# Performance work log

Measured on AMD Instinct MI355X. Metric: run time of the kernel, lower is better.

The kernel has to match this reference:

```python
import jax, jax.numpy as jnp
import numpy as np

B, T, C = 4, 2048, 1024
N_HEAD = 16
HEAD_DIM = C // N_HEAD

def setup_inputs() -> dict:
    key = jax.random.key(0)
    k1, k2, k3 = jax.random.split(key, 3)
    x = jax.random.normal(k1, (B, T, C), dtype=jnp.float32)
    # nn.Linear(C, 3C, bias=False): weight [3C, C], y = x @ W.T
    w_qkv = jax.random.normal(k2, (3 * C, C), dtype=jnp.float32) * (1.0 / np.sqrt(C))
    w_proj = jax.random.normal(k3, (C, C), dtype=jnp.float32) * (1.0 / np.sqrt(C))
    return {"x": x, "w_qkv": w_qkv, "w_proj": w_proj}

def reference(x, w_qkv, w_proj):
    Bx, Tx, Cx = x.shape
    qkv = x @ w_qkv.T  # [B,T,3C]
    q, k, v = jnp.split(qkv, 3, axis=-1)
    def heads(t):
        return t.reshape(Bx, Tx, N_HEAD, HEAD_DIM).transpose(0, 2, 1, 3)  # [B,H,T,D]
    q, k, v = heads(q), heads(k), heads(v)
    scale = HEAD_DIM ** -0.5
    att = jnp.einsum('bhtd,bhsd->bhts', q, k) * scale  # [B,H,T,T]
    causal = jnp.tril(jnp.ones((Tx, Tx), dtype=bool))
    att = jnp.where(causal[None, None], att, -jnp.inf)
    att = jax.nn.softmax(att, axis=-1)
    y = jnp.einsum('bhts,bhsd->bhtd', att, v)  # [B,H,T,D]
    y = y.transpose(0, 2, 1, 3).reshape(Bx, Tx, Cx)
    return y @ w_proj.T
```

## Files before the change

### kernel.cpp

```cpp
#include <hip/hip_runtime.h>
#include <hip/hip_bf16.h>

typedef __attribute__((ext_vector_type(8))) short bf16x8;
typedef __attribute__((ext_vector_type(4))) float f32x4;
typedef __attribute__((ext_vector_type(4))) unsigned short ushort4v;
typedef __attribute__((ext_vector_type(2))) unsigned uint2v;

__device__ __forceinline__ unsigned short f2bf(float f) {
  union { float f; unsigned u; } v; v.f = f;
  unsigned r = v.u + 0x7FFFu + ((v.u >> 16) & 1u);
  return (unsigned short)(r >> 16);
}

__device__ __forceinline__ unsigned pack_bf2(float lo, float hi) {
  __hip_bfloat162 h = __float22bfloat162_rn(make_float2(lo, hi));
  union { __hip_bfloat162 h; unsigned u; } cv; cv.h = h; return cv.u;
}

__device__ __forceinline__ void gll16(const void* g, void* l) {
  __builtin_amdgcn_global_load_lds((const __attribute__((address_space(1))) void*)g,
                                   (__attribute__((address_space(3))) void*)l, 16, 0, 0);
}

#define MFMA16(a, b, c) __builtin_amdgcn_mfma_f32_16x16x32_bf16((a), (b), (c), 0, 0, 0)

__global__ void cvt3(const float* __restrict__ x, const float* __restrict__ wq,
                     const float* __restrict__ wp,
                     unsigned short* __restrict__ xb, unsigned short* __restrict__ wqb,
                     unsigned short* __restrict__ wpb) {
  int i = (blockIdx.x * blockDim.x + threadIdx.x) * 4;
  const float* s; unsigned short* d;
  if (i < 8388608)        { s = x  + i;                 d = xb  + i; }
  else if (i < 11534336)  { s = wq + (i - 8388608);     d = wqb + (i - 8388608); }
  else                    { s = wp + (i - 11534336);    d = wpb + (i - 11534336); }
  float4 f = *(const float4*)s;
  ushort4v r;
  r[0] = f2bf(f.x); r[1] = f2bf(f.y); r[2] = f2bf(f.z); r[3] = f2bf(f.w);
  *(ushort4v*)d = r;
}

template<int EPI, int RPB>
__global__ __launch_bounds__(512, 1)
void gemmp(const unsigned short* __restrict__ A,
           const unsigned short* __restrict__ B,
           unsigned short* __restrict__ obf,
           float* __restrict__ of32,
           int M, int N, int K) {
  extern __shared__ unsigned short lds[];
  const int tid = threadIdx.x, wid = tid >> 6, lane = tid & 63;
  const int c = lane & 15, g = lane >> 4;
  const int wr = wid >> 1, wc = wid & 1;
  const int nbn = N >> 7;
  const int swzbid = (blockIdx.x & 7) * (gridDim.x >> 3) + (blockIdx.x >> 3);
  const int NT = K >> 6;
  const size_t rb = (size_t)K * 2;
  const int sw = (c & 7) << 4;

  const int srow = lane >> 3;
  const int sslot = (lane & 7) ^ srow;
  const char* Abase = (const char*)A;
  const char* Bbase = (const char*)B;

  auto stageA = [&](int m0p, int kt, int par) {
    const char* Agp = Abase + (size_t)(m0p + srow) * rb + sslot * 16 + kt * 128;
#pragma unroll
    for (int j = 0; j < 4; ++j) {
      int ch = wid * 4 + j;
      gll16(Agp + (size_t)(ch * 8) * rb, lds + par * 16384 + ch * 512);
    }
  };
  auto stageB = [&](int n0p, int kt, int par) {
    const char* Bgp = Bbase + (size_t)(n0p + srow) * rb + sslot * 16 + kt * 128;
#pragma unroll
    for (int j = 0; j < 2; ++j) {
      int ch = wid * 2 + j;
      gll16(Bgp + (size_t)(ch * 8) * rb, lds + 32768 + par * 8192 + ch * 512);
    }
  };

  f32x4 acc[4][4];
#pragma unroll
  for (int i = 0; i < 4; ++i)
#pragma unroll
    for (int j = 0; j < 4; ++j) acc[i][j] = f32x4{0.f, 0.f, 0.f, 0.f};

  int m0c = (swzbid / nbn) * 256, n0c = (swzbid % nbn) * 128;

  stageA(m0c, 0, 0); stageB(n0c, 0, 0); stageA(m0c, 1, 1); stageB(n0c, 1, 1);
  asm volatile("s_waitcnt vmcnt(4)" ::: "memory");
  __builtin_amdgcn_s_barrier();

  for (int p = 0; p < RPB; ++p) {
    int m0n = 0, n0n = 0;
    const bool morep = (p + 1 < RPB);
    if (morep) {
      int tile = (p + 1) * gridDim.x + swzbid;
      m0n = (tile / nbn) * 256; n0n = (tile % nbn) * 128;
    }
    for (int t = 0; t < NT; ++t) {
      const int par = t & 1;
      const char* Ac = (const char*)(lds + par * 16384);
      const char* Bc = (const char*)(lds + 32768 + par * 8192);
      bf16x8 af[4][2], bf0[2][2];
#pragma unroll
      for (int mi = 0; mi < 4; ++mi) {
        int arow = wr * 64 + mi * 16 + c;
#pragma unroll
        for (int kk = 0; kk < 2; ++kk)
          af[mi][kk] = *(const bf16x8*)(Ac + arow * 128 + ((kk * 64 + g * 16) ^ sw));
      }
#pragma unroll
      for (int ni = 0; ni < 2; ++ni) {
        int brow = wc * 64 + ni * 16 + c;
#pragma unroll
        for (int kk = 0; kk < 2; ++kk)
          bf0[ni][kk] = *(const bf16x8*)(Bc + brow * 128 + ((kk * 64 + g * 16) ^ sw));
      }
      {
        int tB = t + 1;
        if (tB < NT)      stageB(n0c, tB, tB & 1);
        else if (morep)   stageB(n0n, tB - NT, tB & 1);
      }
      __builtin_amdgcn_s_barrier();
      asm volatile("s_waitcnt lgkmcnt(0)" ::: "memory");
      __builtin_amdgcn_sched_barrier(0);
      __builtin_amdgcn_s_setprio(1);
#pragma unroll
      for (int kk = 0; kk < 2; ++kk)
#pragma unroll
        for (int mi = 0; mi < 4; ++mi)
#pragma unroll
          for (int ni = 0; ni < 2; ++ni)
            acc[mi][ni] = MFMA16(bf0[ni][kk], af[mi][kk], acc[mi][ni]);
      __builtin_amdgcn_s_setprio(0);
      __builtin_amdgcn_s_barrier();
      bf16x8 bf1[2][2];
#pragma unroll
      for (int ni = 0; ni < 2; ++ni) {
        int brow = wc * 64 + (ni + 2) * 16 + c;
#pragma unroll
        for (int kk = 0; kk < 2; ++kk)
          bf1[ni][kk] = *(const bf16x8*)(Bc + brow * 128 + ((kk * 64 + g * 16) ^ sw));
      }
      bool okA;
      {
        int tA = t + 2;
        okA = (tA < NT) || morep;
        if (tA < NT)      stageA(m0c, tA, tA & 1);
        else if (morep)   stageA(m0n, tA - NT, tA & 1);
      }
      __builtin_amdgcn_s_barrier();
      asm volatile("s_waitcnt lgkmcnt(0)" ::: "memory");
      __builtin_amdgcn_sched_barrier(0);
      __builtin_amdgcn_s_setprio(1);
#pragma unroll
      for (int kk = 0; kk < 2; ++kk)
#pragma unroll
        for (int mi = 0; mi < 4; ++mi)
#pragma unroll
          for (int ni = 0; ni < 2; ++ni)
            acc[mi][ni + 2] = MFMA16(bf1[ni][kk], af[mi][kk], acc[mi][ni + 2]);
      __builtin_amdgcn_s_setprio(0);
      if (okA) { asm volatile("s_waitcnt vmcnt(4)" ::: "memory"); }
      else     { asm volatile("s_waitcnt vmcnt(0)" ::: "memory"); }
      __builtin_amdgcn_s_barrier();
    }

#pragma unroll
    for (int mi = 0; mi < 4; ++mi) {
      int mg = m0c + wr * 64 + mi * 16 + c;
      if (EPI == 0) {
        int bb = mg >> 11, tt = mg & 2047;
        size_t rowbase = ((size_t)(bb * 16) * 2048 + tt) * 64;
#pragma unroll
        for (int ni = 0; ni < 4; ++ni) {
          int ng = n0c + wc * 64 + ni * 16 + g * 4;
          int which = ng >> 10, rem = ng & 1023;
          int hh = rem >> 6, dd = rem & 63;
          uint2v pk;
          pk[0] = pack_bf2(acc[mi][ni][0], acc[mi][ni][1]);
          pk[1] = pack_bf2(acc[mi][ni][2], acc[mi][ni][3]);
          *(uint2v*)(obf + (size_t)which * 8388608u + rowbase + (size_t)hh * 131072 + dd) = pk;
        }
      } else {
        float* orow = of32 + (size_t)mg * N + n0c + wc * 64 + g * 4;
#pragma unroll
        for (int ni = 0; ni < 4; ++ni)
          *(f32x4*)(orow + ni * 16) = acc[mi][ni];
      }
    }
#pragma unroll
    for (int i = 0; i < 4; ++i)
#pragma unroll
      for (int j = 0; j < 4; ++j) acc[i][j] = f32x4{0.f, 0.f, 0.f, 0.f};
    m0c = m0n; n0c = n0n;
  }
}

__global__ __launch_bounds__(256, 6)
void attn_fwd(const unsigned short* __restrict__ qb,
              const unsigned short* __restrict__ kb,
              const unsigned short* __restrict__ vb,
              unsigned short* __restrict__ yb) {
  __shared__ unsigned short Kt[64 * 64];
  __shared__ unsigned short Vt[64 * 64];
  __shared__ unsigned short Pl[4 * 16 * 72];
  const int tid = threadIdx.x, w = tid >> 6, lane = tid & 63;
  const int c = lane & 15, g = lane >> 4;
  const int bh = blockIdx.x & 63;
  const int qt = 31 - (blockIdx.x >> 6);
  const int q0 = qt * 64;
  const int b = bh >> 4, h = bh & 15;
  const size_t hb = (size_t)bh * 131072;
  const float GAM = 0.125f * 1.44269504089f;

  const unsigned short* qp = qb + hb + (size_t)(q0 + w * 16 + c) * 64;
  bf16x8 qf0 = *(const bf16x8*)(qp + g * 8);
  bf16x8 qf1 = *(const bf16x8*)(qp + 32 + g * 8);

  f32x4 yacc[4];
#pragma unroll
  for (int i = 0; i < 4; ++i) yacc[i] = f32x4{0.f, 0.f, 0.f, 0.f};
  float mrun = -1e30f, lsum = 0.f;
  unsigned short* pw = Pl + w * (16 * 72);

  for (int kv = 0; kv <= qt; ++kv) {
    const int kv0 = kv * 64;
    const bool diag = (kv == qt);
    if (kv) __syncthreads();
#pragma unroll
    for (int r = 0; r < 2; ++r) {
      int chunk = w * 2 + r;
      int row = chunk * 8 + (lane >> 3);
      int bo = (lane & 7) * 16;
      int sbo = bo ^ ((row & 7) << 4);
      gll16((const char*)(kb + hb + (size_t)(kv0 + row) * 64) + sbo, Kt + chunk * 512);
    }
    {
      int kv2 = (lane & 31) * 2;
      int dblk = w * 16 + (lane >> 5) * 8;
      const unsigned short* vp = vb + hb + (size_t)(kv0 + kv2) * 64 + dblk;
      bf16x8 r0 = *(const bf16x8*)(vp);
      bf16x8 r1 = *(const bf16x8*)(vp + 64);
#pragma unroll
      for (int i = 0; i < 8; ++i) {
        int d = dblk + i;
        unsigned pk2 = ((unsigned)(unsigned short)r0[i]) | (((unsigned)(unsigned short)r1[i]) << 16);
        *(unsigned*)(Vt + d * 64 + (kv2 ^ ((d & 7) << 3))) = pk2;
      }
    }
    __syncthreads();

    f32x4 sacc[4];
#pragma unroll
    for (int nt = 0; nt < 4; ++nt) sacc[nt] = f32x4{0.f, 0.f, 0.f, 0.f};
#pragma unroll
    for (int kk = 0; kk < 2; ++kk)
#pragma unroll
      for (int nt = 0; nt < 4; ++nt) {
        int row = nt * 16 + c;
        bf16x8 kf = *(const bf16x8*)(Kt + row * 64 + ((kk * 32 + g * 8) ^ ((row & 7) << 3)));
        sacc[nt] = MFMA16(kf, (kk ? qf1 : qf0), sacc[nt]);
      }

    if (diag) {
      int ql = w * 16 + c;
#pragma unroll
      for (int nt = 0; nt < 4; ++nt)
#pragma unroll
        for (int r = 0; r < 4; ++r)
          if (nt * 16 + g * 4 + r > ql) sacc[nt][r] = -1e30f;
    }

    float m0 = -1e30f;
#pragma unroll
    for (int nt = 0; nt < 4; ++nt) {
      float a = fmaxf(fmaxf(sacc[nt][0], sacc[nt][1]), fmaxf(sacc[nt][2], sacc[nt][3]));
      m0 = fmaxf(m0, a);
    }
    m0 = fmaxf(m0, __shfl_xor(m0, 16));
    m0 = fmaxf(m0, __shfl_xor(m0, 32));

    if (__any(m0 > mrun + 32.0f)) {
      float mnew = fmaxf(mrun, m0);
      float corr = __builtin_amdgcn_exp2f(GAM * (mrun - mnew));
      lsum *= corr;
#pragma unroll
      for (int dt = 0; dt < 4; ++dt) yacc[dt] *= corr;
      mrun = mnew;
    }

    float bexp = -GAM * mrun;
    float psum = 0.f;
#pragma unroll
    for (int nt = 0; nt < 4; ++nt) {
      float p0 = __builtin_amdgcn_exp2f(fmaf(sacc[nt][0], GAM, bexp));
      float p1 = __builtin_amdgcn_exp2f(fmaf(sacc[nt][1], GAM, bexp));
      float p2 = __builtin_amdgcn_exp2f(fmaf(sacc[nt][2], GAM, bexp));
      float p3 = __builtin_amdgcn_exp2f(fmaf(sacc[nt][3], GAM, bexp));
      psum += (p0 + p1) + (p2 + p3);
      uint2v pkv;
      pkv[0] = pack_bf2(p0, p1);
      pkv[1] = pack_bf2(p2, p3);
      *(uint2v*)(pw + c * 72 + nt * 16 + g * 4) = pkv;
    }
    lsum += psum;

#pragma unroll
    for (int kk = 0; kk < 2; ++kk) {
      bf16x8 pb = *(const bf16x8*)(pw + c * 72 + kk * 32 + g * 8);
#pragma unroll
      for (int dt = 0; dt < 4; ++dt) {
        int n = dt * 16 + c;
        bf16x8 vf = *(const bf16x8*)(Vt + n * 64 + ((kk * 32 + g * 8) ^ ((n & 7) << 3)));
        yacc[dt] = MFMA16(vf, pb, yacc[dt]);
      }
    }
  }

  lsum += __shfl_xor(lsum, 16);
  lsum += __shfl_xor(lsum, 32);
  float inv = 1.0f / lsum;
  int row = q0 + w * 16 + c;
  unsigned short* yp = yb + ((size_t)(b * 2048 + row)) * 1024 + h * 64;
#pragma unroll
  for (int dt = 0; dt < 4; ++dt) {
    uint2v pkv;
    pkv[0] = pack_bf2(yacc[dt][0] * inv, yacc[dt][1] * inv);
    pkv[1] = pack_bf2(yacc[dt][2] * inv, yacc[dt][3] * inv);
    *(uint2v*)(yp + dt * 16 + g * 4) = pkv;
  }
}

extern "C" void kernel_launch(void* const* d_in, const int* in_sizes, int n_in,
                              void* d_out, int out_size, void* d_ws, size_t ws_size,
                              hipStream_t stream) {
  const float* x     = (const float*)d_in[0];
  const float* wqkv  = (const float*)d_in[1];
  const float* wproj = (const float*)d_in[2];
  float* out = (float*)d_out;

  unsigned short* ws     = (unsigned short*)d_ws;
  unsigned short* xb     = ws;
  unsigned short* wqkvb  = xb + 8388608;
  unsigned short* wprojb = wqkvb + 3145728;
  unsigned short* qkvb   = wprojb + 1048576;
  unsigned short* yb     = qkvb + 3 * 8388608;

  cvt3<<<12288, 256, 0, stream>>>(x, wqkv, wproj, xb, wqkvb, wprojb);

  gemmp<0, 3><<<256, 512, 98304, stream>>>(xb, wqkvb, qkvb, nullptr, 8192, 3072, 1024);
  attn_fwd<<<2048, 256, 0, stream>>>(qkvb, qkvb + 8388608, qkvb + 2 * 8388608, yb);
  gemmp<1, 1><<<256, 512, 98304, stream>>>(yb, wprojb, nullptr, out, 8192, 1024, 1024);
}
```

Baseline: 173.2 us.

## Process 128 query rows per attention block to reuse K/V tiles

The attention kernel now handles a 128-row query tile per block. Each wave owns two 16-row sub-tiles, so every K/V tile loaded into LDS feeds twice as many MFMAs, and the grid shrinks from 2048 to 1024 blocks. Causal masking becomes per sub-tile, and sub-tiles that lie entirely above the diagonal are skipped. The cost is more registers per wave (launch bounds lowered to 4 waves), a larger P buffer in LDS, fewer blocks for load balancing, and some idle waves on diagonal tiles.

Measured after the change: 178.0 us. 2.7% more time.

```diff
diff --git a/kernel.cpp b/kernel.cpp
--- a/kernel.cpp
+++ b/kernel.cpp
@@ -197,36 +197,43 @@
   }
 }
 
-__global__ __launch_bounds__(256, 6)
+__global__ __launch_bounds__(256, 4)
 void attn_fwd(const unsigned short* __restrict__ qb,
               const unsigned short* __restrict__ kb,
               const unsigned short* __restrict__ vb,
               unsigned short* __restrict__ yb) {
   __shared__ unsigned short Kt[64 * 64];
   __shared__ unsigned short Vt[64 * 64];
-  __shared__ unsigned short Pl[4 * 16 * 72];
+  __shared__ unsigned short Pl[4 * 32 * 72];
   const int tid = threadIdx.x, w = tid >> 6, lane = tid & 63;
   const int c = lane & 15, g = lane >> 4;
   const int bh = blockIdx.x & 63;
-  const int qt = 31 - (blockIdx.x >> 6);
-  const int q0 = qt * 64;
+  const int qt = 15 - (blockIdx.x >> 6);
+  const int q0 = qt * 128;
   const int b = bh >> 4, h = bh & 15;
   const size_t hb = (size_t)bh * 131072;
   const float GAM = 0.125f * 1.44269504089f;
 
-  const unsigned short* qp = qb + hb + (size_t)(q0 + w * 16 + c) * 64;
-  bf16x8 qf0 = *(const bf16x8*)(qp + g * 8);
-  bf16x8 qf1 = *(const bf16x8*)(qp + 32 + g * 8);
-
-  f32x4 yacc[4];
-#pragma unroll
-  for (int i = 0; i < 4; ++i) yacc[i] = f32x4{0.f, 0.f, 0.f, 0.f};
-  float mrun = -1e30f, lsum = 0.f;
-  unsigned short* pw = Pl + w * (16 * 72);
-
-  for (int kv = 0; kv <= qt; ++kv) {
+  bf16x8 qf[2][2];
+#pragma unroll
+  for (int s = 0; s < 2; ++s) {
+    const unsigned short* qp = qb + hb + (size_t)(q0 + w * 32 + s * 16 + c) * 64;
+    qf[s][0] = *(const bf16x8*)(qp + g * 8);
+    qf[s][1] = *(const bf16x8*)(qp + 32 + g * 8);
+  }
+
+  f32x4 yacc[2][4];
+#pragma unroll
+  for (int s = 0; s < 2; ++s)
+#pragma unroll
+    for (int i = 0; i < 4; ++i) yacc[s][i] = f32x4{0.f, 0.f, 0.f, 0.f};
+  float mrun[2] = {-1e30f, -1e30f};
+  float lsum[2] = {0.f, 0.f};
+  unsigned short* pw = Pl + w * (32 * 72);
+
+  const int nkv = 2 * qt + 2;
+  for (int kv = 0; kv < nkv; ++kv) {
     const int kv0 = kv * 64;
-    const bool diag = (kv == qt);
     if (kv) __syncthreads();
 #pragma unroll
     for (int r = 0; r < 2; ++r) {
@@ -251,84 +258,88 @@
     }
     __syncthreads();
 
-    f32x4 sacc[4];
-#pragma unroll
-    for (int nt = 0; nt < 4; ++nt) sacc[nt] = f32x4{0.f, 0.f, 0.f, 0.f};
-#pragma unroll
-    for (int kk = 0; kk < 2; ++kk)
+#pragma unroll
+    for (int s = 0; s < 2; ++s) {
+      const int rowmin = q0 + w * 32 + s * 16;
+      if (kv0 > rowmin + 15) continue;
+      f32x4 sacc[4];
+#pragma unroll
+      for (int nt = 0; nt < 4; ++nt) sacc[nt] = f32x4{0.f, 0.f, 0.f, 0.f};
+#pragma unroll
+      for (int kk = 0; kk < 2; ++kk)
+#pragma unroll
+        for (int nt = 0; nt < 4; ++nt) {
+          int row = nt * 16 + c;
+          bf16x8 kf = *(const bf16x8*)(Kt + row * 64 + ((kk * 32 + g * 8) ^ ((row & 7) << 3)));
+          sacc[nt] = MFMA16(kf, qf[s][kk], sacc[nt]);
+        }
+      if (kv0 + 63 > rowmin) {
+        int ql = rowmin + c;
+#pragma unroll
+        for (int nt = 0; nt < 4; ++nt)
+#pragma unroll
+          for (int r = 0; r < 4; ++r)
+            if (kv0 + nt * 16 + g * 4 + r > ql) sacc[nt][r] = -1e30f;
+      }
+      float m0 = -1e30f;
 #pragma unroll
       for (int nt = 0; nt < 4; ++nt) {
-        int row = nt * 16 + c;
-        bf16x8 kf = *(const bf16x8*)(Kt + row * 64 + ((kk * 32 + g * 8) ^ ((row & 7) << 3)));
-        sacc[nt] = MFMA16(kf, (kk ? qf1 : qf0), sacc[nt]);
-      }
-
-    if (diag) {
-      int ql = w * 16 + c;
-#pragma unroll
-      for (int nt = 0; nt < 4; ++nt)
-#pragma unroll
-        for (int r = 0; r < 4; ++r)
-          if (nt * 16 + g * 4 + r > ql) sacc[nt][r] = -1e30f;
-    }
-
-    float m0 = -1e30f;
-#pragma unroll
-    for (int nt = 0; nt < 4; ++nt) {
-      float a = fmaxf(fmaxf(sacc[nt][0], sacc[nt][1]), fmaxf(sacc[nt][2], sacc[nt][3]));
-      m0 = fmaxf(m0, a);
-    }
-    m0 = fmaxf(m0, __shfl_xor(m0, 16));
-    m0 = fmaxf(m0, __shfl_xor(m0, 32));
-
-    if (__any(m0 > mrun + 32.0f)) {
-      float mnew = fmaxf(mrun, m0);
-      float corr = __builtin_amdgcn_exp2f(GAM * (mrun - mnew));
-      lsum *= corr;
-#pragma unroll
-      for (int dt = 0; dt < 4; ++dt) yacc[dt] *= corr;
-      mrun = mnew;
-    }
-
-    float bexp = -GAM * mrun;
-    float psum = 0.f;
-#pragma unroll
-    for (int nt = 0; nt < 4; ++nt) {
-      float p0 = __builtin_amdgcn_exp2f(fmaf(sacc[nt][0], GAM, bexp));
-      float p1 = __builtin_amdgcn_exp2f(fmaf(sacc[nt][1], GAM, bexp));
-      float p2 = __builtin_amdgcn_exp2f(fmaf(sacc[nt][2], GAM, bexp));
-      float p3 = __builtin_amdgcn_exp2f(fmaf(sacc[nt][3], GAM, bexp));
-      psum += (p0 + p1) + (p2 + p3);
+        float a = fmaxf(fmaxf(sacc[nt][0], sacc[nt][1]), fmaxf(sacc[nt][2], sacc[nt][3]));
+        m0 = fmaxf(m0, a);
+      }
+      m0 = fmaxf(m0, __shfl_xor(m0, 16));
+      m0 = fmaxf(m0, __shfl_xor(m0, 32));
+      if (__any(m0 > mrun[s] + 32.0f)) {
+        float mnew = fmaxf(mrun[s], m0);
+        float corr = __builtin_amdgcn_exp2f(GAM * (mrun[s] - mnew));
+        lsum[s] *= corr;
+#pragma unroll
+        for (int dt = 0; dt < 4; ++dt) yacc[s][dt] *= corr;
+        mrun[s] = mnew;
+      }
+      float bexp = -GAM * mrun[s];
+      float psum = 0.f;
+#pragma unroll
+      for (int nt = 0; nt < 4; ++nt) {
+        float p0 = __builtin_amdgcn_exp2f(fmaf(sacc[nt][0], GAM, bexp));
+        float p1 = __builtin_amdgcn_exp2f(fmaf(sacc[nt][1], GAM, bexp));
+        float p2 = __builtin_amdgcn_exp2f(fmaf(sacc[nt][2], GAM, bexp));
+        float p3 = __builtin_amdgcn_exp2f(fmaf(sacc[nt][3], GAM, bexp));
+        psum += (p0 + p1) + (p2 + p3);
+        uint2v pkv;
+        pkv[0] = pack_bf2(p0, p1);
+        pkv[1] = pack_bf2(p2, p3);
+        *(uint2v*)(pw + (s * 16 + c) * 72 + nt * 16 + g * 4) = pkv;
+      }
+      lsum[s] += psum;
+#pragma unroll
+      for (int kk = 0; kk < 2; ++kk) {
+        bf16x8 pb = *(const bf16x8*)(pw + (s * 16 + c) * 72 + kk * 32 + g * 8);
+#pragma unroll
+        for (int dt = 0; dt < 4; ++dt) {
+          int n = dt * 16 + c;
+          bf16x8 vf = *(const bf16x8*)(Vt + n * 64 + ((kk * 32 + g * 8) ^ ((n & 7) << 3)));
+          yacc[s][dt] = MFMA16(vf, pb, yacc[s][dt]);
+        }
+      }
+    }
+  }
+
+#pragma unroll
+  for (int s = 0; s < 2; ++s) {
+    float ls = lsum[s];
+    ls += __shfl_xor(ls, 16);
+    ls += __shfl_xor(ls, 32);
+    float inv = 1.0f / ls;
+    int row = q0 + w * 32 + s * 16 + c;
+    unsigned short* yp = yb + ((size_t)(b * 2048 + row)) * 1024 + h * 64;
+#pragma unroll
+    for (int dt = 0; dt < 4; ++dt) {
       uint2v pkv;
-      pkv[0] = pack_bf2(p0, p1);
-      pkv[1] = pack_bf2(p2, p3);
-      *(uint2v*)(pw + c * 72 + nt * 16 + g * 4) = pkv;
-    }
-    lsum += psum;
-
-#pragma unroll
-    for (int kk = 0; kk < 2; ++kk) {
-      bf16x8 pb = *(const bf16x8*)(pw + c * 72 + kk * 32 + g * 8);
-#pragma unroll
-      for (int dt = 0; dt < 4; ++dt) {
-        int n = dt * 16 + c;
-        bf16x8 vf = *(const bf16x8*)(Vt + n * 64 + ((kk * 32 + g * 8) ^ ((n & 7) << 3)));
-        yacc[dt] = MFMA16(vf, pb, yacc[dt]);
-      }
-    }
-  }
-
-  lsum += __shfl_xor(lsum, 16);
-  lsum += __shfl_xor(lsum, 32);
-  float inv = 1.0f / lsum;
-  int row = q0 + w * 16 + c;
-  unsigned short* yp = yb + ((size_t)(b * 2048 + row)) * 1024 + h * 64;
-#pragma unroll
-  for (int dt = 0; dt < 4; ++dt) {
-    uint2v pkv;
-    pkv[0] = pack_bf2(yacc[dt][0] * inv, yacc[dt][1] * inv);
-    pkv[1] = pack_bf2(yacc[dt][2] * inv, yacc[dt][3] * inv);
-    *(uint2v*)(yp + dt * 16 + g * 4) = pkv;
+      pkv[0] = pack_bf2(yacc[s][dt][0] * inv, yacc[s][dt][1] * inv);
+      pkv[1] = pack_bf2(yacc[s][dt][2] * inv, yacc[s][dt][3] * inv);
+      *(uint2v*)(yp + dt * 16 + g * 4) = pkv;
+    }
   }
 }
 
@@ -350,6 +361,6 @@
   cvt3<<<12288, 256, 0, stream>>>(x, wqkv, wproj, xb, wqkvb, wprojb);
 
   gemmp<0, 3><<<256, 512, 98304, stream>>>(xb, wqkvb, qkvb, nullptr, 8192, 3072, 1024);
-  attn_fwd<<<2048, 256, 0, stream>>>(qkvb, qkvb + 8388608, qkvb + 2 * 8388608, yb);
+  attn_fwd<<<1024, 256, 0, stream>>>(qkvb, qkvb + 8388608, qkvb + 2 * 8388608, yb);
   gemmp<1, 1><<<256, 512, 98304, stream>>>(yb, wprojb, nullptr, out, 8192, 1024, 1024);
 }
```
